# Performance work log

Hardware: AMD Instinct MI355X
Metric: run time of the kernel (lower is better)

## Reference

```python
import jax, jax.numpy as jnp
import numpy as np

B, S, D, H, DFF = 2, 2048, 768, 12, 2048
DK = D // H
EPS = 1e-6


def setup_inputs() -> dict:
    key = jax.random.key(0)
    ks = jax.random.split(key, 16)
    sd = 0.02
    inp = {
        "x": jax.random.normal(ks[0], (B, S, D), jnp.float32),
        "mask": jnp.ones((B, 1, S), jnp.int32),
        "Wq": jax.random.normal(ks[1], (D, D), jnp.float32) * sd,
        "bq": jnp.zeros((D,), jnp.float32),
        "Wk": jax.random.normal(ks[2], (D, D), jnp.float32) * sd,
        "bk": jnp.zeros((D,), jnp.float32),
        "Wv": jax.random.normal(ks[3], (D, D), jnp.float32) * sd,
        "bv": jnp.zeros((D,), jnp.float32),
        "Wo": jax.random.normal(ks[4], (D, D), jnp.float32) * sd,
        "bo": jnp.zeros((D,), jnp.float32),
        "W1": jax.random.normal(ks[5], (DFF, D), jnp.float32) * sd,
        "b1": jnp.zeros((DFF,), jnp.float32),
        "W2": jax.random.normal(ks[6], (D, DFF), jnp.float32) * sd,
        "b2": jnp.zeros((D,), jnp.float32),
        "alpha": jnp.ones((D,), jnp.float32),
        "beta": jnp.zeros((D,), jnp.float32),
    }
    return inp


def _norm(x, alpha, beta):
    # Matches torch Norm: std with Bessel correction (ddof=1), eps added to std.
    mu = jnp.mean(x, axis=-1, keepdims=True)
    sd = jnp.std(x, axis=-1, keepdims=True, ddof=1)
    return alpha * (x - mu) / (sd + EPS) + beta


def reference(x, mask, Wq, bq, Wk, bk, Wv, bv, Wo, bo, W1, b1, W2, b2, alpha, beta):
    # --- pre-norm MHA block ---
    n = _norm(x, alpha, beta)
    q = (n @ Wq.T + bq).reshape(B, S, H, DK).transpose(0, 2, 1, 3)  # [B,H,S,DK]
    k = (n @ Wk.T + bk).reshape(B, S, H, DK).transpose(0, 2, 1, 3)
    v = (n @ Wv.T + bv).reshape(B, S, H, DK).transpose(0, 2, 1, 3)
    scores = jnp.einsum("bhqd,bhkd->bhqk", q, k) / jnp.sqrt(jnp.float32(DK))
    # mask: [B,1,S] -> unsqueeze(1) -> [B,1,1,S], broadcast over heads & query rows
    scores = jnp.where(mask[:, None, :, :] == 0, jnp.float32(-1e9), scores)
    attn = jax.nn.softmax(scores, axis=-1)
    # dropout is identity in eval mode
    ctx = jnp.einsum("bhqk,bhkd->bhqd", attn, v)  # [B,H,S,DK]
    concat = ctx.transpose(0, 2, 1, 3).reshape(B, S, D)
    x = x + (concat @ Wo.T + bo)
    # --- pre-norm FFN block (same shared Norm params) ---
    n2 = _norm(x, alpha, beta)
    h = jax.nn.relu(n2 @ W1.T + b1)
    x = x + (h @ W2.T + b2)
    return x
```

## Files before the change

### kernel.cpp

```cpp
#include <hip/hip_runtime.h>

#define SS   2048
#define DD   768
#define HH   12
#define DFFF 2048
#define BSR  4096
#define QKV_LD 2304

typedef __attribute__((ext_vector_type(8))) short bf16x8;
typedef __attribute__((ext_vector_type(4))) float f32x4;

__device__ __forceinline__ unsigned short f2b(float f) {
  union { float f; unsigned u; } x; x.f = f;
  unsigned r = (x.u + 0x7FFFu + ((x.u >> 16) & 1u)) >> 16;
  return (unsigned short)r;
}

__device__ __forceinline__ unsigned cvtpk(float lo, float hi) {
  unsigned r;
  asm("v_cvt_pk_bf16_f32 %0, %1, %2" : "=v"(r) : "v"(lo), "v"(hi));
  return r;
}

__device__ __forceinline__ void gload_lds16(const void* g, void* l) {
  __builtin_amdgcn_global_load_lds(
      (const __attribute__((address_space(1))) unsigned int*)g,
      (__attribute__((address_space(3))) unsigned int*)l,
      16, 0, 0);
}

__device__ __forceinline__ unsigned lds_u32(const void* p) {
  return (unsigned)(unsigned long long)p;
}

__device__ __forceinline__ void ln_row(const float* __restrict__ xr,
                                       const float* __restrict__ alpha,
                                       const float* __restrict__ beta,
                                       unsigned short* __restrict__ orow, int lane) {
  float4 v[3];
#pragma unroll
  for (int g = 0; g < 3; ++g) v[g] = *(const float4*)&xr[lane * 12 + g * 4];
  float sum = 0.f;
#pragma unroll
  for (int g = 0; g < 3; ++g) sum += v[g].x + v[g].y + v[g].z + v[g].w;
#pragma unroll
  for (int off = 1; off < 64; off <<= 1) sum += __shfl_xor(sum, off);
  float mu = sum * (1.0f / 768.0f);
  float ss = 0.f;
#pragma unroll
  for (int g = 0; g < 3; ++g) {
    float a0 = v[g].x - mu, a1 = v[g].y - mu, a2 = v[g].z - mu, a3 = v[g].w - mu;
    ss += a0 * a0 + a1 * a1 + a2 * a2 + a3 * a3;
  }
#pragma unroll
  for (int off = 1; off < 64; off <<= 1) ss += __shfl_xor(ss, off);
  float sd = sqrtf(ss * (1.0f / 767.0f));
  float inv = 1.0f / (sd + 1e-6f);
#pragma unroll
  for (int g = 0; g < 3; ++g) {
    float4 al = *(const float4*)&alpha[lane * 12 + g * 4];
    float4 be = *(const float4*)&beta[lane * 12 + g * 4];
    uint2 pk;
    pk.x = cvtpk(al.x * (v[g].x - mu) * inv + be.x, al.y * (v[g].y - mu) * inv + be.y);
    pk.y = cvtpk(al.z * (v[g].z - mu) * inv + be.z, al.w * (v[g].w - mu) * inv + be.w);
    *(uint2*)&orow[lane * 12 + g * 4] = pk;
  }
}

__global__ __launch_bounds__(256) void pre_k(const float* __restrict__ Wq,
                                             const float* __restrict__ Wk,
                                             const float* __restrict__ Wv,
                                             const float* __restrict__ Wo,
                                             const float* __restrict__ W1,
                                             const float* __restrict__ W2,
                                             const float* __restrict__ bq,
                                             const float* __restrict__ bk,
                                             const float* __restrict__ bv,
                                             const float* __restrict__ x,
                                             const float* __restrict__ alpha,
                                             const float* __restrict__ beta,
                                             unsigned short* __restrict__ wqkv,
                                             unsigned short* __restrict__ wo_b,
                                             unsigned short* __restrict__ w1_b,
                                             unsigned short* __restrict__ w2_b,
                                             float* __restrict__ bqkv,
                                             unsigned short* __restrict__ n_b) {
  const int blk = blockIdx.x;
  const float* src;
  unsigned short* dst;
  long off;
  if (blk < 1728) {
    int r = blk / 576;
    src = r == 0 ? Wq : r == 1 ? Wk : Wv;
    dst = wqkv + (long)r * 589824;
    off = (long)(blk - r * 576) * 1024 + threadIdx.x * 4;
  } else if (blk < 2304) {
    src = Wo; dst = wo_b; off = (long)(blk - 1728) * 1024 + threadIdx.x * 4;
  } else if (blk < 3840) {
    src = W1; dst = w1_b; off = (long)(blk - 2304) * 1024 + threadIdx.x * 4;
  } else if (blk < 5376) {
    src = W2; dst = w2_b; off = (long)(blk - 3840) * 1024 + threadIdx.x * 4;
  } else if (blk == 5376) {
    for (int k = threadIdx.x; k < 2304; k += 256)
      bqkv[k] = k < 768 ? bq[k] : k < 1536 ? bk[k - 768] : bv[k - 1536];
    return;
  } else {
    int row = (blk - 5377) * 4 + (threadIdx.x >> 6);
    ln_row(x + (long)row * DD, alpha, beta, n_b + (long)row * DD, threadIdx.x & 63);
    return;
  }
  float4 v = *(const float4*)&src[off];
  uint2 pk;
  pk.x = cvtpk(v.x, v.y);
  pk.y = cvtpk(v.z, v.w);
  *(uint2*)&dst[off] = pk;
}

__global__ __launch_bounds__(256) void layernorm_k(const float* __restrict__ x,
                                                   const float* __restrict__ alpha,
                                                   const float* __restrict__ beta,
                                                   unsigned short* __restrict__ outb) {
  int row = blockIdx.x * 4 + (threadIdx.x >> 6);
  ln_row(x + (long)row * DD, alpha, beta, outb + (long)row * DD, threadIdx.x & 63);
}

template <int BM, int BN, bool RELU, bool RES, bool OUTB, bool QSC>
__global__ __launch_bounds__(256, (BM == 64 || BN == 64) ? 4 : 3)
void gemm_bt(const unsigned short* __restrict__ A,
             const unsigned short* __restrict__ W,
             const float* __restrict__ bias,
             const float* __restrict__ res,
             void* __restrict__ outp,
             int M, int N, int K) {
  __shared__ __align__(16) unsigned short As[BM * 64];
  __shared__ __align__(16) unsigned short Bs[BN * 64];
  constexpr int MF = BM / 32;
  constexpr int NF = BN / 32;
  const int t = threadIdx.x;
  const int lane = t & 63;
  const int w = t >> 6;
  const int wr = w >> 1, wc = w & 1;
  const int l15 = lane & 15, l4 = lane >> 4;
  const int nwg = gridDim.x * gridDim.y;
  const int lin = blockIdx.y * gridDim.x + blockIdx.x;
  const int u2 = (lin & 7) * (nwg >> 3) + (lin >> 3);
  const long brow = (long)(u2 / gridDim.x) * BM;
  const long bcol = (long)(u2 % gridDim.x) * BN;
  f32x4 acc[MF][NF] = {};
  const int r0 = t >> 3;
  const int c8s = (((t & 7) ^ (r0 & 7)) & 7) * 8;
  const int rd_swz = (l15 & 7) << 4;

  for (int k0 = 0; k0 < K; k0 += 64) {
    __syncthreads();
#pragma unroll
    for (int p = 0; p < BM / 32; ++p)
      gload_lds16(&A[(brow + p * 32 + r0) * (long)K + k0 + c8s],
                  (char*)As + p * 4096 + w * 1024);
#pragma unroll
    for (int p = 0; p < BN / 32; ++p)
      gload_lds16(&W[(bcol + p * 32 + r0) * (long)K + k0 + c8s],
                  (char*)Bs + p * 4096 + w * 1024);
    __syncthreads();
#pragma unroll
    for (int ks = 0; ks < 2; ++ks) {
      bf16x8 a[MF], b[NF];
#pragma unroll
      for (int m = 0; m < MF; ++m)
        a[m] = *(const bf16x8*)((const char*)As +
                                (wr * (BM / 2) + m * 16 + l15) * 128 +
                                ((ks * 64 + l4 * 16) ^ rd_swz));
#pragma unroll
      for (int n = 0; n < NF; ++n)
        b[n] = *(const bf16x8*)((const char*)Bs +
                                (wc * (BN / 2) + n * 16 + l15) * 128 +
                                ((ks * 64 + l4 * 16) ^ rd_swz));
#pragma unroll
      for (int m = 0; m < MF; ++m)
#pragma unroll
        for (int n = 0; n < NF; ++n)
          acc[m][n] = __builtin_amdgcn_mfma_f32_16x16x32_bf16(a[m], b[n], acc[m][n], 0, 0, 0);
    }
  }
#pragma unroll
  for (int n = 0; n < NF; ++n) {
    const long col = bcol + wc * (BN / 2) + n * 16 + l15;
    const float bv = bias[col];
    const float sc = (QSC && col < 768) ? 0.18033688f : 1.0f;
#pragma unroll
    for (int m = 0; m < MF; ++m) {
      const long row0 = brow + wr * (BM / 2) + m * 16 + l4 * 4;
#pragma unroll
      for (int r = 0; r < 4; ++r) {
        float v = acc[m][n][r] + bv;
        if (RELU) v = fmaxf(v, 0.0f);
        if (QSC) v *= sc;
        long o = (row0 + r) * (long)N + col;
        if (RES) v += res[o];
        if (OUTB) ((unsigned short*)outp)[o] = f2b(v);
        else ((float*)outp)[o] = v;
      }
    }
  }
}

__global__ __launch_bounds__(256, 3) void attn_kernel(const unsigned short* __restrict__ qkv,
                                                      const int* __restrict__ mask,
                                                      unsigned short* __restrict__ ctx) {
  __shared__ __align__(16) unsigned short Ks[2][64 * 64];
  __shared__ __align__(16) unsigned short Vt[3][64 * 64];
  const int t = threadIdx.x, lane = t & 63, w = t >> 6;
  const int l15 = lane & 15, l4 = lane >> 4;
  const int u = (blockIdx.x & 7) * 96 + (blockIdx.x >> 3);
  const int qt = u & 31;
  const int h = (u >> 5) % 12;
  const int b = u / 384;
  const long rowB = (long)b * SS;

  unsigned bm;
  {
    int* tfl = (int*)&Vt[0][0];
    const int* mb = &mask[b * SS + t * 8];
    int4 a0 = *(const int4*)mb;
    int4 a1 = *(const int4*)(mb + 4);
    int allv = (a0.x && a0.y && a0.z && a0.w && a1.x && a1.y && a1.z && a1.w) ? 1 : 0;
    allv &= __shfl_xor(allv, 1);
    allv &= __shfl_xor(allv, 2);
    allv &= __shfl_xor(allv, 4);
    if ((t & 7) == 0) tfl[t >> 3] = allv;
    __syncthreads();
    int vv = (lane < 32) ? tfl[lane] : 1;
    bm = (unsigned)__ballot(vv);
    __syncthreads();
  }

  bf16x8 aq[2];
#pragma unroll
  for (int ks = 0; ks < 2; ++ks)
    aq[ks] = *(const bf16x8*)&qkv[(rowB + qt * 64 + w * 16 + l15) * QKV_LD +
                                  h * 64 + ks * 32 + l4 * 8];

  const int krow = w * 8 + (lane >> 3);
  const int kdo = (((lane & 7) ^ (lane >> 3)) & 7) << 3;
  const unsigned short* kgbase = &qkv[(rowB + krow) * QKV_LD + 768 + h * 64 + kdo];
  const int kread_swz = (l15 & 7) << 4;

  const unsigned short* vsrc[2];
#pragma unroll
  for (int p = 0; p < 2; ++p) {
    int X = p * 4096 + w * 1024 + lane * 16;
    int d_blk = X >> 11;
    int rem = X & 2047;
    int k_blk = rem >> 7;
    int krw = (rem >> 5) & 3;
    int c = (rem >> 4) & 1;
    int vkey = k_blk * 4 + krw;
    int vd0 = d_blk * 16 + c * 8;
    vsrc[p] = &qkv[(rowB + vkey) * QKV_LD + 1536 + h * 64 + vd0];
  }
  const unsigned vtrl = (unsigned)(l15 * 2 + l4 * 128);
  unsigned vad0 = lds_u32(&Vt[0][0]) + vtrl;
  unsigned vad1 = lds_u32(&Vt[1][0]) + vtrl;
  unsigned vad2 = lds_u32(&Vt[2][0]) + vtrl;
  char* vdst0 = (char*)&Vt[2][0];
  char* vdst1 = (char*)&Vt[0][0];
  char* vdst2 = (char*)&Vt[1][0];
  const char* kread = (const char*)&Ks[1][0];
  char* kdst = (char*)&Ks[0][0];

  union { unsigned uu[4]; bf16x8 b8; } vone;
  vone.uu[0] = vone.uu[1] = vone.uu[2] = vone.uu[3] = 0x3F803F80u;

  f32x4 o[4] = {};
  f32x4 o4 = {};
  float mrun = -1e30f;
  f32x4 sp[4];

#define QK_INTO(dst, kbase)                                                     \
  { __builtin_amdgcn_s_setprio(1);                                             \
    _Pragma("unroll") for (int ks = 0; ks < 2; ++ks)                           \
    _Pragma("unroll") for (int cg = 0; cg < 4; ++cg) {                         \
      bf16x8 ak = *(const bf16x8*)((kbase) + (cg * 16 + l15) * 128 +           \
                                   ((ks * 64 + l4 * 16) ^ kread_swz));         \
      dst[cg] = __builtin_amdgcn_mfma_f32_16x16x32_bf16(ak, aq[ks], dst[cg], 0, 0, 0); \
    }                                                                           \
    __builtin_amdgcn_s_setprio(0); }

#define MASK_APPLY(dst, kb)                                                     \
  if (__builtin_expect(!((bm >> (kb)) & 1), 0)) {                              \
    const int* mb2 = &mask[b * SS + (kb) * 64 + l4 * 4];                       \
    _Pragma("unroll") for (int cg = 0; cg < 4; ++cg) {                         \
      int4 mm = *(const int4*)(mb2 + cg * 16);                                 \
      int mi[4] = {mm.x, mm.y, mm.z, mm.w};                                    \
      _Pragma("unroll") for (int r = 0; r < 4; ++r)                            \
        dst[cg][r] += mi[r] ? 0.f : -1.44269504e9f;                            \
    } }

#pragma unroll
  for (int p = 0; p < 2; ++p)
    gload_lds16(kgbase + (long)p * 32 * QKV_LD, (char*)&Ks[0][0] + p * 4096 + w * 1024);
#pragma unroll
  for (int p = 0; p < 2; ++p)
    gload_lds16(vsrc[p], (char*)&Vt[0][0] + p * 4096 + w * 1024);
  __syncthreads();
#pragma unroll
  for (int p = 0; p < 2; ++p)
    gload_lds16(kgbase + ((long)64 + p * 32) * QKV_LD, (char*)&Ks[1][0] + p * 4096 + w * 1024);
#pragma unroll
  for (int p = 0; p < 2; ++p)
    gload_lds16(vsrc[p] + (long)64 * QKV_LD, (char*)&Vt[1][0] + p * 4096 + w * 1024);
#pragma unroll
  for (int cg = 0; cg < 4; ++cg) sp[cg] = f32x4{0.f, 0.f, 0.f, 0.f};
  QK_INTO(sp, (const char*)&Ks[0][0]);
  MASK_APPLY(sp, 0);

  for (int i = 0; i < 31; ++i) {
    __syncthreads();
    if (i < 30) {
#pragma unroll
      for (int p = 0; p < 2; ++p)
        gload_lds16(kgbase + ((long)(i + 2) * 64 + p * 32) * QKV_LD,
                    kdst + p * 4096 + w * 1024);
#pragma unroll
      for (int p = 0; p < 2; ++p)
        gload_lds16(vsrc[p] + (long)(i + 2) * 64 * QKV_LD,
                    vdst0 + p * 4096 + w * 1024);
    }
    f32x4 sc[4] = {};
    QK_INTO(sc, kread);
    MASK_APPLY(sc, i + 1);
    {
      float t0 = fmaxf(fmaxf(sp[0][0], sp[0][1]), sp[0][2]);
      float t1 = fmaxf(fmaxf(sp[0][3], sp[1][0]), sp[1][1]);
      float t2 = fmaxf(fmaxf(sp[1][2], sp[1][3]), sp[2][0]);
      float t3 = fmaxf(fmaxf(sp[2][1], sp[2][2]), sp[2][3]);
      float t4 = fmaxf(fmaxf(sp[3][0], sp[3][1]), sp[3][2]);
      float t5 = fmaxf(fmaxf(t0, t1), t2);
      float t6 = fmaxf(fmaxf(t3, t4), sp[3][3]);
      float pmax = fmaxf(t5, t6);
      pmax = fmaxf(pmax, __shfl_xor(pmax, 16));
      pmax = fmaxf(pmax, __shfl_xor(pmax, 32));
      if (!__all(pmax <= mrun + 8.0f)) {
        float mnew = fmaxf(mrun, pmax);
        float fac = __builtin_amdgcn_exp2f(mrun - mnew);
#pragma unroll
        for (int mg = 0; mg < 4; ++mg)
#pragma unroll
          for (int r = 0; r < 4; ++r) o[mg][r] *= fac;
#pragma unroll
        for (int r = 0; r < 4; ++r) o4[r] *= fac;
        mrun = mnew;
      }
#pragma unroll
      for (int cg = 0; cg < 4; ++cg)
#pragma unroll
        for (int r = 0; r < 4; ++r)
          sp[cg][r] = __builtin_amdgcn_exp2f(sp[cg][r] - mrun);
    }
    __builtin_amdgcn_s_setprio(1);
#pragma unroll
    for (int ks = 0; ks < 2; ++ks) {
      union { unsigned uu[4]; bf16x8 b8; } bp;
      bp.uu[0] = cvtpk(sp[2 * ks][0], sp[2 * ks][1]);
      bp.uu[1] = cvtpk(sp[2 * ks][2], sp[2 * ks][3]);
      bp.uu[2] = cvtpk(sp[2 * ks + 1][0], sp[2 * ks + 1][1]);
      bp.uu[3] = cvtpk(sp[2 * ks + 1][2], sp[2 * ks + 1][3]);
      uint2 q0, q1, q2, q3, q4, q5, q6, q7;
      if (ks == 0) {
        asm volatile(
            "ds_read_b64_tr_b16 %0, %8 offset:0\n\t"
            "ds_read_b64_tr_b16 %1, %8 offset:512\n\t"
            "ds_read_b64_tr_b16 %2, %8 offset:2048\n\t"
            "ds_read_b64_tr_b16 %3, %8 offset:2560\n\t"
            "ds_read_b64_tr_b16 %4, %8 offset:4096\n\t"
            "ds_read_b64_tr_b16 %5, %8 offset:4608\n\t"
            "ds_read_b64_tr_b16 %6, %8 offset:6144\n\t"
            "ds_read_b64_tr_b16 %7, %8 offset:6656\n\t"
            "s_waitcnt lgkmcnt(0)"
            : "=&v"(q0), "=&v"(q1), "=&v"(q2), "=&v"(q3),
              "=&v"(q4), "=&v"(q5), "=&v"(q6), "=&v"(q7)
            : "v"(vad0));
      } else {
        asm volatile(
            "ds_read_b64_tr_b16 %0, %8 offset:1024\n\t"
            "ds_read_b64_tr_b16 %1, %8 offset:1536\n\t"
            "ds_read_b64_tr_b16 %2, %8 offset:3072\n\t"
            "ds_read_b64_tr_b16 %3, %8 offset:3584\n\t"
            "ds_read_b64_tr_b16 %4, %8 offset:5120\n\t"
            "ds_read_b64_tr_b16 %5, %8 offset:5632\n\t"
            "ds_read_b64_tr_b16 %6, %8 offset:7168\n\t"
            "ds_read_b64_tr_b16 %7, %8 offset:7680\n\t"
            "s_waitcnt lgkmcnt(0)"
            : "=&v"(q0), "=&v"(q1), "=&v"(q2), "=&v"(q3),
              "=&v"(q4), "=&v"(q5), "=&v"(q6), "=&v"(q7)
            : "v"(vad0));
      }
      union { uint2 u2[2]; bf16x8 b8; } av0, av1, av2, av3;
      av0.u2[0] = q0; av0.u2[1] = q1;
      av1.u2[0] = q2; av1.u2[1] = q3;
      av2.u2[0] = q4; av2.u2[1] = q5;
      av3.u2[0] = q6; av3.u2[1] = q7;
      o[0] = __builtin_amdgcn_mfma_f32_16x16x32_bf16(av0.b8, bp.b8, o[0], 0, 0, 0);
      o[1] = __builtin_amdgcn_mfma_f32_16x16x32_bf16(av1.b8, bp.b8, o[1], 0, 0, 0);
      o[2] = __builtin_amdgcn_mfma_f32_16x16x32_bf16(av2.b8, bp.b8, o[2], 0, 0, 0);
      o[3] = __builtin_amdgcn_mfma_f32_16x16x32_bf16(av3.b8, bp.b8, o[3], 0, 0, 0);
      o4 = __builtin_amdgcn_mfma_f32_16x16x32_bf16(vone.b8, bp.b8, o4, 0, 0, 0);
    }
    __builtin_amdgcn_s_setprio(0);
#pragma unroll
    for (int cg = 0; cg < 4; ++cg) sp[cg] = sc[cg];
    { const char* tk = kread; kread = kdst; kdst = (char*)tk; }
    { unsigned tv = vad0; vad0 = vad1; vad1 = vad2; vad2 = tv; }
    { char* td = vdst0; vdst0 = vdst1; vdst1 = vdst2; vdst2 = td; }
  }

  {
    float t0 = fmaxf(fmaxf(sp[0][0], sp[0][1]), sp[0][2]);
    float t1 = fmaxf(fmaxf(sp[0][3], sp[1][0]), sp[1][1]);
    float t2 = fmaxf(fmaxf(sp[1][2], sp[1][3]), sp[2][0]);
    float t3 = fmaxf(fmaxf(sp[2][1], sp[2][2]), sp[2][3]);
    float t4 = fmaxf(fmaxf(sp[3][0], sp[3][1]), sp[3][2]);
    float t5 = fmaxf(fmaxf(t0, t1), t2);
    float t6 = fmaxf(fmaxf(t3, t4), sp[3][3]);
    float pmax = fmaxf(t5, t6);
    pmax = fmaxf(pmax, __shfl_xor(pmax, 16));
    pmax = fmaxf(pmax, __shfl_xor(pmax, 32));
    if (!__all(pmax <= mrun + 8.0f)) {
      float mnew = fmaxf(mrun, pmax);
      float fac = __builtin_amdgcn_exp2f(mrun - mnew);
#pragma unroll
      for (int mg = 0; mg < 4; ++mg)
#pragma unroll
        for (int r = 0; r < 4; ++r) o[mg][r] *= fac;
#pragma unroll
      for (int r = 0; r < 4; ++r) o4[r] *= fac;
      mrun = mnew;
    }
#pragma unroll
    for (int cg = 0; cg < 4; ++cg)
#pragma unroll
      for (int r = 0; r < 4; ++r)
        sp[cg][r] = __builtin_amdgcn_exp2f(sp[cg][r] - mrun);
#pragma unroll
    for (int ks = 0; ks < 2; ++ks) {
      union { unsigned uu[4]; bf16x8 b8; } bp;
      bp.uu[0] = cvtpk(sp[2 * ks][0], sp[2 * ks][1]);
      bp.uu[1] = cvtpk(sp[2 * ks][2], sp[2 * ks][3]);
      bp.uu[2] = cvtpk(sp[2 * ks + 1][0], sp[2 * ks + 1][1]);
      bp.uu[3] = cvtpk(sp[2 * ks + 1][2], sp[2 * ks + 1][3]);
      uint2 q0, q1, q2, q3, q4, q5, q6, q7;
      if (ks == 0) {
        asm volatile(
            "ds_read_b64_tr_b16 %0, %8 offset:0\n\t"
            "ds_read_b64_tr_b16 %1, %8 offset:512\n\t"
            "ds_read_b64_tr_b16 %2, %8 offset:2048\n\t"
            "ds_read_b64_tr_b16 %3, %8 offset:2560\n\t"
            "ds_read_b64_tr_b16 %4, %8 offset:4096\n\t"
            "ds_read_b64_tr_b16 %5, %8 offset:4608\n\t"
            "ds_read_b64_tr_b16 %6, %8 offset:6144\n\t"
            "ds_read_b64_tr_b16 %7, %8 offset:6656\n\t"
            "s_waitcnt lgkmcnt(0)"
            : "=&v"(q0), "=&v"(q1), "=&v"(q2), "=&v"(q3),
              "=&v"(q4), "=&v"(q5), "=&v"(q6), "=&v"(q7)
            : "v"(vad0));
      } else {
        asm volatile(
            "ds_read_b64_tr_b16 %0, %8 offset:1024\n\t"
            "ds_read_b64_tr_b16 %1, %8 offset:1536\n\t"
            "ds_read_b64_tr_b16 %2, %8 offset:3072\n\t"
            "ds_read_b64_tr_b16 %3, %8 offset:3584\n\t"
            "ds_read_b64_tr_b16 %4, %8 offset:5120\n\t"
            "ds_read_b64_tr_b16 %5, %8 offset:5632\n\t"
            "ds_read_b64_tr_b16 %6, %8 offset:7168\n\t"
            "ds_read_b64_tr_b16 %7, %8 offset:7680\n\t"
            "s_waitcnt lgkmcnt(0)"
            : "=&v"(q0), "=&v"(q1), "=&v"(q2), "=&v"(q3),
              "=&v"(q4), "=&v"(q5), "=&v"(q6), "=&v"(q7)
            : "v"(vad0));
      }
      union { uint2 u2[2]; bf16x8 b8; } av0, av1, av2, av3;
      av0.u2[0] = q0; av0.u2[1] = q1;
      av1.u2[0] = q2; av1.u2[1] = q3;
      av2.u2[0] = q4; av2.u2[1] = q5;
      av3.u2[0] = q6; av3.u2[1] = q7;
      o[0] = __builtin_amdgcn_mfma_f32_16x16x32_bf16(av0.b8, bp.b8, o[0], 0, 0, 0);
      o[1] = __builtin_amdgcn_mfma_f32_16x16x32_bf16(av1.b8, bp.b8, o[1], 0, 0, 0);
      o[2] = __builtin_amdgcn_mfma_f32_16x16x32_bf16(av2.b8, bp.b8, o[2], 0, 0, 0);
      o[3] = __builtin_amdgcn_mfma_f32_16x16x32_bf16(av3.b8, bp.b8, o[3], 0, 0, 0);
      o4 = __builtin_amdgcn_mfma_f32_16x16x32_bf16(vone.b8, bp.b8, o4, 0, 0, 0);
    }
  }
#undef QK_INTO
#undef MASK_APPLY

  const float inv = 1.0f / o4[0];
  const long obase = (rowB + qt * 64 + w * 16 + l15) * DD + h * 64 + l4 * 4;
#pragma unroll
  for (int mg = 0; mg < 4; ++mg) {
    *(unsigned*)&ctx[obase + mg * 16] = cvtpk(o[mg][0] * inv, o[mg][1] * inv);
    *(unsigned*)&ctx[obase + mg * 16 + 2] = cvtpk(o[mg][2] * inv, o[mg][3] * inv);
  }
}

static const size_t OFF_WQKV = 0;
static const size_t OFF_WO = 3538944;
static const size_t OFF_W1 = 4718592;
static const size_t OFF_W2 = 7864320;
static const size_t OFF_BQKV = 11010048;
static const size_t OFF_N = 11019264;
static const size_t OFF_QKV = 17310720;
static const size_t OFF_CTX = 36185088;
static const size_t OFF_X1 = 42476544;

extern "C" void kernel_launch(void* const* d_in, const int* in_sizes, int n_in,
                              void* d_out, int out_size, void* d_ws, size_t ws_size,
                              hipStream_t stream) {
  (void)in_sizes; (void)n_in; (void)out_size; (void)ws_size;
  const float* x = (const float*)d_in[0];
  const int* mask = (const int*)d_in[1];
  const float* Wq = (const float*)d_in[2];
  const float* bq = (const float*)d_in[3];
  const float* Wk = (const float*)d_in[4];
  const float* bk = (const float*)d_in[5];
  const float* Wv = (const float*)d_in[6];
  const float* bv = (const float*)d_in[7];
  const float* Wo = (const float*)d_in[8];
  const float* bo = (const float*)d_in[9];
  const float* W1 = (const float*)d_in[10];
  const float* b1 = (const float*)d_in[11];
  const float* W2 = (const float*)d_in[12];
  const float* b2 = (const float*)d_in[13];
  const float* alpha = (const float*)d_in[14];
  const float* beta = (const float*)d_in[15];

  char* ws = (char*)d_ws;
  unsigned short* wqkv = (unsigned short*)(ws + OFF_WQKV);
  unsigned short* wo_b = (unsigned short*)(ws + OFF_WO);
  unsigned short* w1_b = (unsigned short*)(ws + OFF_W1);
  unsigned short* w2_b = (unsigned short*)(ws + OFF_W2);
  float* bqkv = (float*)(ws + OFF_BQKV);
  unsigned short* n_b = (unsigned short*)(ws + OFF_N);
  unsigned short* qkv_b = (unsigned short*)(ws + OFF_QKV);
  unsigned short* h_b = qkv_b;
  unsigned short* ctx_b = (unsigned short*)(ws + OFF_CTX);
  float* x1_f = (float*)(ws + OFF_X1);
  float* out_f = (float*)d_out;

  pre_k<<<6401, 256, 0, stream>>>(Wq, Wk, Wv, Wo, W1, W2, bq, bk, bv,
                                  x, alpha, beta, wqkv, wo_b, w1_b, w2_b, bqkv, n_b);
  gemm_bt<128, 128, false, false, true, true><<<dim3(18, 32), 256, 0, stream>>>(
      n_b, wqkv, bqkv, nullptr, qkv_b, BSR, QKV_LD, DD);
  attn_kernel<<<768, 256, 0, stream>>>(qkv_b, mask, ctx_b);
  gemm_bt<64, 64, false, true, false, false><<<dim3(12, 64), 256, 0, stream>>>(
      ctx_b, wo_b, bo, x, x1_f, BSR, DD, DD);
  layernorm_k<<<1024, 256, 0, stream>>>(x1_f, alpha, beta, n_b);
  gemm_bt<64, 128, true, false, true, false><<<dim3(16, 64), 256, 0, stream>>>(
      n_b, w1_b, b1, nullptr, h_b, BSR, DFFF, DD);
  gemm_bt<64, 64, false, true, false, false><<<dim3(12, 64), 256, 0, stream>>>(
      h_b, w2_b, b2, x1_f, out_f, BSR, DD, DFFF);
}
```

Baseline: 135.3 us.

## Move Wo/W1/W2 bf16 conversion into extra attention blocks to overlap

Drops the Wo, W1 and W2 fp32-to-bf16 conversion from the prologue kernel and runs it instead in 228 extra blocks appended to the attention launch, each converting 16K elements. The aim is to hide this memory-bound conversion behind the compute-bound attention blocks rather than paying for it serially before the QKV GEMM. The attention launch bound also rises from 3 to 4 waves per SIMD, which may force register spilling. The extra blocks compete for CUs with the attention tiles.

Measured after the change: 132.9 us. No clear change (-1.8%).

```diff
diff --git a/kernel.cpp b/kernel.cpp
--- a/kernel.cpp
+++ b/kernel.cpp
@@ -70,9 +70,6 @@
 __global__ __launch_bounds__(256) void pre_k(const float* __restrict__ Wq,
                                              const float* __restrict__ Wk,
                                              const float* __restrict__ Wv,
-                                             const float* __restrict__ Wo,
-                                             const float* __restrict__ W1,
-                                             const float* __restrict__ W2,
                                              const float* __restrict__ bq,
                                              const float* __restrict__ bk,
                                              const float* __restrict__ bv,
@@ -80,40 +77,26 @@
                                              const float* __restrict__ alpha,
                                              const float* __restrict__ beta,
                                              unsigned short* __restrict__ wqkv,
-                                             unsigned short* __restrict__ wo_b,
-                                             unsigned short* __restrict__ w1_b,
-                                             unsigned short* __restrict__ w2_b,
                                              float* __restrict__ bqkv,
                                              unsigned short* __restrict__ n_b) {
   const int blk = blockIdx.x;
-  const float* src;
-  unsigned short* dst;
-  long off;
   if (blk < 1728) {
     int r = blk / 576;
-    src = r == 0 ? Wq : r == 1 ? Wk : Wv;
-    dst = wqkv + (long)r * 589824;
-    off = (long)(blk - r * 576) * 1024 + threadIdx.x * 4;
-  } else if (blk < 2304) {
-    src = Wo; dst = wo_b; off = (long)(blk - 1728) * 1024 + threadIdx.x * 4;
-  } else if (blk < 3840) {
-    src = W1; dst = w1_b; off = (long)(blk - 2304) * 1024 + threadIdx.x * 4;
-  } else if (blk < 5376) {
-    src = W2; dst = w2_b; off = (long)(blk - 3840) * 1024 + threadIdx.x * 4;
-  } else if (blk == 5376) {
+    const float* src = r == 0 ? Wq : r == 1 ? Wk : Wv;
+    unsigned short* dst = wqkv + (long)r * 589824;
+    long off = (long)(blk - r * 576) * 1024 + threadIdx.x * 4;
+    float4 v = *(const float4*)&src[off];
+    uint2 pk;
+    pk.x = cvtpk(v.x, v.y);
+    pk.y = cvtpk(v.z, v.w);
+    *(uint2*)&dst[off] = pk;
+  } else if (blk == 1728) {
     for (int k = threadIdx.x; k < 2304; k += 256)
       bqkv[k] = k < 768 ? bq[k] : k < 1536 ? bk[k - 768] : bv[k - 1536];
-    return;
   } else {
-    int row = (blk - 5377) * 4 + (threadIdx.x >> 6);
+    int row = (blk - 1729) * 4 + (threadIdx.x >> 6);
     ln_row(x + (long)row * DD, alpha, beta, n_b + (long)row * DD, threadIdx.x & 63);
-    return;
-  }
-  float4 v = *(const float4*)&src[off];
-  uint2 pk;
-  pk.x = cvtpk(v.x, v.y);
-  pk.y = cvtpk(v.z, v.w);
-  *(uint2*)&dst[off] = pk;
+  }
 }
 
 __global__ __launch_bounds__(256) void layernorm_k(const float* __restrict__ x,
@@ -204,9 +187,35 @@
   }
 }
 
-__global__ __launch_bounds__(256, 3) void attn_kernel(const unsigned short* __restrict__ qkv,
+__global__ __launch_bounds__(256, 4) void attn_kernel(const unsigned short* __restrict__ qkv,
                                                       const int* __restrict__ mask,
-                                                      unsigned short* __restrict__ ctx) {
+                                                      unsigned short* __restrict__ ctx,
+                                                      const float* __restrict__ Wo,
+                                                      const float* __restrict__ W1,
+                                                      const float* __restrict__ W2,
+                                                      unsigned short* __restrict__ wo_b,
+                                                      unsigned short* __restrict__ w1_b,
+                                                      unsigned short* __restrict__ w2_b) {
+  if (blockIdx.x >= 768) {
+    const long base = (long)(blockIdx.x - 768) * 16384 + threadIdx.x * 4;
+#pragma unroll 4
+    for (int i = 0; i < 16; ++i) {
+      long e = base + i * 1024;
+      const float* s;
+      unsigned short* d;
+      long off;
+      if (e < 589824) { s = Wo; d = wo_b; off = e; }
+      else if (e < 2162688) { s = W1; d = w1_b; off = e - 589824; }
+      else { s = W2; d = w2_b; off = e - 2162688; }
+      float4 v = *(const float4*)&s[off];
+      uint2 pk;
+      pk.x = cvtpk(v.x, v.y);
+      pk.y = cvtpk(v.z, v.w);
+      *(uint2*)&d[off] = pk;
+    }
+    return;
+  }
+
   __shared__ __align__(16) unsigned short Ks[2][64 * 64];
   __shared__ __align__(16) unsigned short Vt[3][64 * 64];
   const int t = threadIdx.x, lane = t & 63, w = t >> 6;
@@ -546,11 +555,12 @@
   float* x1_f = (float*)(ws + OFF_X1);
   float* out_f = (float*)d_out;
 
-  pre_k<<<6401, 256, 0, stream>>>(Wq, Wk, Wv, Wo, W1, W2, bq, bk, bv,
-                                  x, alpha, beta, wqkv, wo_b, w1_b, w2_b, bqkv, n_b);
+  pre_k<<<2753, 256, 0, stream>>>(Wq, Wk, Wv, bq, bk, bv,
+                                  x, alpha, beta, wqkv, bqkv, n_b);
   gemm_bt<128, 128, false, false, true, true><<<dim3(18, 32), 256, 0, stream>>>(
       n_b, wqkv, bqkv, nullptr, qkv_b, BSR, QKV_LD, DD);
-  attn_kernel<<<768, 256, 0, stream>>>(qkv_b, mask, ctx_b);
+  attn_kernel<<<996, 256, 0, stream>>>(qkv_b, mask, ctx_b,
+                                       Wo, W1, W2, wo_b, w1_b, w2_b);
   gemm_bt<64, 64, false, true, false, false><<<dim3(12, 64), 256, 0, stream>>>(
       ctx_b, wo_b, bo, x, x1_f, BSR, DD, DD);
   layernorm_k<<<1024, 256, 0, stream>>>(x1_f, alpha, beta, n_b);
```
